# Optimization experiments

Measured on AMD Instinct MI355X. Metric: run time of the kernel, lower is better.

## Reference

```python
import jax, jax.numpy as jnp
import numpy as np

THRESHOLD = 16.0
BN_EPS = 1e-5


def setup_inputs() -> dict:
    key = jax.random.key(0)
    k_x, k_w, k_b, k_g, k_be = jax.random.split(key, 5)
    B, C, H, W = 4, 128, 64, 64
    C2 = 128
    x = jax.random.normal(k_x, (B, C, H, W), dtype=jnp.float32)
    # nn.Linear(c1, c2): weight [c2, c1], bias [c2]
    W_fc = jax.random.normal(k_w, (C2, C), dtype=jnp.float32) * (1.0 / np.sqrt(C))
    b_fc = jax.random.normal(k_b, (C2,), dtype=jnp.float32) * 0.01
    # BatchNorm2d affine params
    gamma = jnp.ones((C2,), dtype=jnp.float32) + 0.1 * jax.random.normal(k_g, (C2,), dtype=jnp.float32)
    beta = 0.1 * jax.random.normal(k_be, (C2,), dtype=jnp.float32)
    return {"x": x, "W_fc": W_fc, "b_fc": b_fc, "gamma": gamma, "beta": beta}


def reference(x, W_fc, b_fc, gamma, beta):
    b, c, h, w = x.shape
    xf = x.reshape(b, c, h * w).transpose(0, 2, 1)  # [B, N, C]

    # torch.cdist(feature, feature): pairwise L2 distances [B, N, N]
    sq = jnp.sum(xf * xf, axis=-1)  # [B, N]
    d2 = sq[:, :, None] + sq[:, None, :] - 2.0 * jnp.einsum('bic,bjc->bij', xf, xf)
    dist = jnp.sqrt(jnp.maximum(d2, 0.0))
    incidence = (dist < THRESHOLD).astype(x.dtype)  # [B, N, N], N vertices x N hyperedges

    # HyPConv: fc then vertex->edge (mean) then edge->vertex (mean)
    xe = jnp.einsum('bnc,dc->bnd', xf, W_fc) + b_fc  # [B, N, c2]

    # v2e: path = incidence^T (dims 1,2); mean over incident vertices
    deg_e = jnp.sum(incidence, axis=1)  # [B, N] = row-sums of incidence^T
    edge = jnp.einsum('bve,bvc->bec', incidence, xe)  # incidence^T @ xe
    edge = jnp.where(deg_e > 0, 1.0 / deg_e, 0.0)[:, :, None] * edge

    # e2v: path = incidence; mean over incident hyperedges
    deg_v = jnp.sum(incidence, axis=2)  # [B, N]
    vert = jnp.einsum('bve,bec->bvc', incidence, edge)
    vert = jnp.where(deg_v > 0, 1.0 / deg_v, 0.0)[:, :, None] * vert

    # residual is Identity (c1 == c2)
    out = vert + xf  # [B, N, c2]
    out = out.transpose(0, 2, 1).reshape(b, -1, h, w)  # [B, c2, H, W]

    # BatchNorm2d in training mode (batch statistics, biased variance)
    mean = jnp.mean(out, axis=(0, 2, 3))
    var = jnp.var(out, axis=(0, 2, 3))
    y = (out - mean[None, :, None, None]) * jax.lax.rsqrt(var[None, :, None, None] + BN_EPS)
    y = gamma[None, :, None, None] * y + beta[None, :, None, None]
    return y * jax.nn.sigmoid(y)  # SiLU
```

## Files before the change

kernel.cpp:

```cpp
#include <hip/hip_runtime.h>
#include <hip/hip_bf16.h>

#define NB 4
#define CH 128
#define NN 4096

typedef short bf16x8 __attribute__((ext_vector_type(8)));
typedef float f32x4 __attribute__((ext_vector_type(4)));
typedef float f32x16 __attribute__((ext_vector_type(16)));
using u16 = unsigned short;
using u32 = unsigned int;

__device__ __forceinline__ u16 f2bf(float v) {
  return __builtin_bit_cast(u16, __float2bfloat16(v));
}
__device__ __forceinline__ float bf2f(u16 u) {
  return __builtin_bit_cast(float, ((u32)u) << 16);
}

__device__ __forceinline__ void gld16(const void* g, void* l) {
  __builtin_amdgcn_global_load_lds((const __attribute__((address_space(1))) void*)g,
                                   (__attribute__((address_space(3))) void*)l,
                                   16, 0, 0);
}

__global__ void k_wbt(const float* __restrict__ W, u16* __restrict__ WbT) {
  int t = blockIdx.x * 256 + threadIdx.x;
  int c = t >> 7, d = t & 127;
  WbT[c * 128 + d] = f2bf(W[d * 128 + c]);
}

__global__ __launch_bounds__(256) void k_prep(const float* __restrict__ x,
                                              u16* __restrict__ xfb,
                                              float* __restrict__ sq) {
  __shared__ float ls[128][65];
  int blk = blockIdx.x;
  int b = blk >> 6;
  int n0 = (blk & 63) * 64;
  int t = threadIdx.x;
  const float* xb = x + (size_t)b * CH * NN;
  {
    int j = t & 63, cb = t >> 6;
#pragma unroll
    for (int i = 0; i < 32; ++i) {
      int c = cb * 32 + i;
      ls[c][j] = xb[(size_t)c * NN + n0 + j];
    }
  }
  __syncthreads();
  int jr = t >> 2, q = t & 3;
  float s = 0.f;
  u16* dst = xfb + ((size_t)b * NN + n0 + jr) * CH + q * 32;
#pragma unroll
  for (int ch = 0; ch < 4; ++ch) {
    u32 w[4];
#pragma unroll
    for (int p = 0; p < 4; ++p) {
      float va = ls[q * 32 + ch * 8 + 2 * p][jr];
      float vb = ls[q * 32 + ch * 8 + 2 * p + 1][jr];
      s += va * va + vb * vb;
      w[p] = (u32)f2bf(va) | ((u32)f2bf(vb) << 16);
    }
    ((uint4*)dst)[ch] = make_uint4(w[0], w[1], w[2], w[3]);
  }
  s += __shfl_xor(s, 1);
  s += __shfl_xor(s, 2);
  if (q == 0) sq[b * NN + n0 + jr] = s;
}

__global__ __launch_bounds__(256) void k_pack(const u16* __restrict__ xfb,
                                              const float* __restrict__ sq,
                                              u16* __restrict__ XA,
                                              u16* __restrict__ XG) {
  int bid = blockIdx.x;
  int b = bid >> 7, vt = bid & 127;
  int t = threadIdx.x;
  int v = t >> 3, q = t & 7;
  int row = vt * 32 + v;
  const u16* src = xfb + ((size_t)b * NN + row) * CH;
  size_t tb = ((size_t)b * 128 + vt) * 4608;
  float sv = sq[b * NN + row];
  u16 shi = f2bf(sv);
  u16 slo = f2bf(sv - bf2f(shi));
  const u32 one = 0x3F80u;
  for (int slot = q; slot < 18; slot += 8) {
    int k9 = slot >> 1, h = slot & 1;
    int dsto = (slot * 32 + v) * 8;
    uint4 pa, pg;
    if (k9 < 8) {
      pa = *(const uint4*)(src + k9 * 16 + h * 8);
      u32 w4[4] = {pa.x, pa.y, pa.z, pa.w};
      u32 g4[4];
#pragma unroll
      for (int p = 0; p < 4; ++p) {
        u16 lo = (u16)(w4[p] & 0xFFFF), hi16 = (u16)(w4[p] >> 16);
        u16 glo = f2bf(-2.f * bf2f(lo));
        u16 ghi = f2bf(-2.f * bf2f(hi16));
        g4[p] = (u32)glo | ((u32)ghi << 16);
      }
      pg = make_uint4(g4[0], g4[1], g4[2], g4[3]);
    } else {
      if (h == 0) {
        pa = make_uint4((u32)shi | ((u32)slo << 16), one | (one << 16), 0u, 0u);
        pg = make_uint4(one | (one << 16), (u32)shi | ((u32)slo << 16), 0u, 0u);
      } else {
        pa = make_uint4(0u, 0u, 0u, 0u);
        pg = pa;
      }
    }
    *(uint4*)(XA + tb + dsto) = pa;
    *(uint4*)(XG + tb + dsto) = pg;
  }
}

__global__ __launch_bounds__(256) void k_xe(const u16* __restrict__ xfb,
                                            const u16* __restrict__ WbT,
                                            const float* __restrict__ bfc,
                                            u16* __restrict__ XE2) {
  __shared__ char sm[65536];
  float* lsX = (float*)sm;
  u16* lsW = (u16*)(sm + 32768);
  int blk = blockIdx.x;  int b = blk >> 6;  int n0 = (blk & 63) * 64;
  int t = threadIdx.x;
  {
    int n = t >> 2, q = t & 3;
    const uint4* s4 = (const uint4*)(xfb + ((size_t)b * NN + n0 + n) * CH + q * 32);
    float* dstf = lsX + n * 128 + q * 32;
#pragma unroll
    for (int ch = 0; ch < 4; ++ch) {
      uint4 pk = s4[ch];
      u32 vals[4] = {pk.x, pk.y, pk.z, pk.w};
#pragma unroll
      for (int p = 0; p < 4; ++p) {
        dstf[ch * 8 + 2 * p]     = __builtin_bit_cast(float, vals[p] << 16);
        dstf[ch * 8 + 2 * p + 1] = __builtin_bit_cast(float, vals[p] & 0xFFFF0000u);
      }
    }
  }
  {
    int c = t >> 1, half = t & 1;
    const uint4* s = (const uint4*)(WbT + c * 128 + half * 64);
    uint4* d = (uint4*)(lsW + c * 128 + half * 64);
#pragma unroll
    for (int i = 0; i < 8; ++i) d[i] = s[i];
  }
  __syncthreads();
  int d = t & 127, ng = t >> 7;
  float acc[32];
  float bias = bfc[d];
#pragma unroll
  for (int n = 0; n < 32; ++n) acc[n] = bias;
  for (int c4 = 0; c4 < 32; ++c4) {
    float wv[4];
#pragma unroll
    for (int p = 0; p < 4; ++p) wv[p] = bf2f(lsW[(c4 * 4 + p) * 128 + d]);
#pragma unroll
    for (int n = 0; n < 32; ++n) {
      f32x4 xv = *(const f32x4*)(lsX + (ng * 32 + n) * 128 + c4 * 4);
      acc[n] = fmaf(xv[0], wv[0], acc[n]);
      acc[n] = fmaf(xv[1], wv[1], acc[n]);
      acc[n] = fmaf(xv[2], wv[2], acc[n]);
      acc[n] = fmaf(xv[3], wv[3], acc[n]);
    }
  }
  __syncthreads();
  u16* lsO = (u16*)sm;
#pragma unroll
  for (int n = 0; n < 32; ++n) lsO[d * 64 + ng * 32 + n] = f2bf(acc[n]);
  __syncthreads();
  {
    size_t tbv = ((size_t)b * 128 + (n0 >> 5));
#pragma unroll
    for (int it = 0; it < 4; ++it) {
      int cid = t + it * 256;
      int vtl = cid >> 9, g = cid & 511;
      int dloc = g & 31, hi2 = (g >> 5) & 1, h = (g >> 6) & 1, dt = g >> 7;
      int rowd = dt * 32 + dloc;
      int nl = vtl * 32 + h * 16 + hi2 * 8;
      *(uint4*)(XE2 + ((tbv + vtl) * 512 + g) * 8) = *(const uint4*)(lsO + rowd * 64 + nl);
    }
  }
}

__global__ __launch_bounds__(256, 2) void k_hyp(const u16* __restrict__ XAg,
                                                const u16* __restrict__ XGg,
                                                const u16* __restrict__ B2g,
                                                u16* __restrict__ outP,
                                                float* __restrict__ deg,
                                                int dodeg) {
  __shared__ __align__(16) char smem[34816];
  int t = threadIdx.x;
  int lane = t & 63, w = t >> 6;
  int r = lane & 31, hi = lane >> 5;
  int bid = blockIdx.x;
  int b = bid >> 7, rem = bid & 127;
  int et = rem >> 2, ks = rem & 3;
  int e0 = et * 128;
  int vt0 = ks * 32;

  bf16x8 B1[9];
  {
    const u16* g = XGg + ((size_t)(b * 128 + et * 4 + w)) * 4608 + (hi * 32 + r) * 8;
#pragma unroll
    for (int k9 = 0; k9 < 9; ++k9) B1[k9] = *(const bf16x8*)(g + k9 * 512);
  }

  f32x16 acc2[4];
#pragma unroll
  for (int dt = 0; dt < 4; ++dt)
#pragma unroll
    for (int q = 0; q < 16; ++q) acc2[dt][q] = 0.f;
  float dg = 0.f;

  const u16* xa_t = XAg + ((size_t)(b * 128 + vt0)) * 4608;
  const u16* b2_t = B2g + ((size_t)(b * 128 + vt0)) * 4096;

  {
    char* L = smem;
    for (int i = w; i < 9; i += 4) gld16(xa_t + i * 512 + lane * 8, L + i * 1024);
    for (int i = w; i < 8; i += 4) gld16(b2_t + i * 512 + lane * 8, L + 9216 + i * 1024);
  }
  __syncthreads();
  int cur = 0;
  for (int tile = 0; tile < 32; ++tile) {
    if (tile + 1 < 32) {
      char* L = smem + (cur ^ 1) * 17408;
      const u16* ga = xa_t + (size_t)(tile + 1) * 4608;
      const u16* gb = b2_t + (size_t)(tile + 1) * 4096;
      for (int i = w; i < 9; i += 4) gld16(ga + i * 512 + lane * 8, L + i * 1024);
      for (int i = w; i < 8; i += 4) gld16(gb + i * 512 + lane * 8, L + 9216 + i * 1024);
    }
    char* LA = smem + cur * 17408;
    char* LB = LA + 9216;
    f32x16 d2;
    {
      bf16x8 a1 = *(const bf16x8*)(LA + lane * 16);
      f32x16 z;
#pragma unroll
      for (int q = 0; q < 16; ++q) z[q] = 0.f;
      d2 = __builtin_amdgcn_mfma_f32_32x32x16_bf16(a1, B1[0], z, 0, 0, 0);
    }
#pragma unroll
    for (int k9 = 1; k9 < 9; ++k9) {
      bf16x8 a1 = *(const bf16x8*)(LA + k9 * 1024 + lane * 16);
      d2 = __builtin_amdgcn_mfma_f32_32x32x16_bf16(a1, B1[k9], d2, 0, 0, 0);
    }
    float p[16];
#pragma unroll
    for (int q = 0; q < 16; ++q) {
      p[q] = (d2[q] < 256.f) ? 1.f : 0.f;
      dg += p[q];
    }
    u32 c[8];
#pragma unroll
    for (int pr = 0; pr < 8; ++pr)
      asm("v_cvt_pk_bf16_f32 %0, %1, %2" : "=v"(c[pr]) : "v"(p[2 * pr]), "v"(p[2 * pr + 1]));
    asm volatile("v_permlane32_swap_b32 %0, %1" : "+v"(c[0]), "+v"(c[2]));
    asm volatile("v_permlane32_swap_b32 %0, %1" : "+v"(c[1]), "+v"(c[3]));
    asm volatile("v_permlane32_swap_b32 %0, %1" : "+v"(c[4]), "+v"(c[6]));
    asm volatile("v_permlane32_swap_b32 %0, %1" : "+v"(c[5]), "+v"(c[7]));
    uint4 u0 = make_uint4(c[0], c[1], c[2], c[3]);
    uint4 u1 = make_uint4(c[4], c[5], c[6], c[7]);
    bf16x8 A2h0 = __builtin_bit_cast(bf16x8, u0);
    bf16x8 A2h1 = __builtin_bit_cast(bf16x8, u1);
#pragma unroll
    for (int dt = 0; dt < 4; ++dt) {
      bf16x8 b20 = *(const bf16x8*)(LB + dt * 2048 + hi * 512 + r * 16);
      bf16x8 b21 = *(const bf16x8*)(LB + dt * 2048 + 1024 + hi * 512 + r * 16);
      acc2[dt] = __builtin_amdgcn_mfma_f32_32x32x16_bf16(A2h0, b20, acc2[dt], 0, 0, 0);
      acc2[dt] = __builtin_amdgcn_mfma_f32_32x32x16_bf16(A2h1, b21, acc2[dt], 0, 0, 0);
    }
    __syncthreads();
    cur ^= 1;
  }
  if (dodeg) {
    float dtot = dg + __shfl_xor(dg, 32);
    if (hi == 0) atomicAdd(&deg[b * NN + e0 + w * 32 + r], dtot);
  }
  {
    u16* lsE = (u16*)smem + w * 4096;
#pragma unroll
    for (int dt = 0; dt < 4; ++dt)
#pragma unroll
      for (int q = 0; q < 16; ++q) {
        int e_l = (q & 3) + 8 * (q >> 2) + 4 * hi;
        lsE[e_l * 128 + dt * 32 + r] = f2bf(acc2[dt][q]);
      }
  }
  __syncthreads();
  {
    uint4* g4 = (uint4*)(outP + ((size_t)(ks * NB + b) * NN + e0) * 128);
    const uint4* l4 = (const uint4*)smem;
#pragma unroll
    for (int i = 0; i < 8; ++i) g4[t + i * 256] = l4[t + i * 256];
  }
}

__global__ __launch_bounds__(256) void k_escale(const u16* __restrict__ P,
                                                const float* __restrict__ deg,
                                                u16* __restrict__ ED2) {
  int bid = blockIdx.x;
  int b = bid >> 7, et = bid & 127;
  int t = threadIdx.x;
#pragma unroll
  for (int c2 = 0; c2 < 2; ++c2) {
    int g = t + c2 * 256;
    int dloc = g & 31, hi2 = (g >> 5) & 1, h = (g >> 6) & 1, dt = g >> 7;
    int d = dt * 32 + dloc;
    int ebase = et * 32 + h * 16 + hi2 * 8;
    u16 outv[8];
#pragma unroll
    for (int j = 0; j < 8; ++j) {
      int e = ebase + j;
      size_t idx = ((size_t)b * NN + e) * 128 + d;
      float s = bf2f(P[idx]) + bf2f(P[idx + 2097152]) +
                bf2f(P[idx + 2 * 2097152]) + bf2f(P[idx + 3 * 2097152]);
      float dv = deg[b * NN + e];
      float f = dv > 0.f ? 1.0f / dv : 0.f;
      outv[j] = f2bf(s * f);
    }
    *(uint4*)(ED2 + (((size_t)b * 128 + et) * 512 + g) * 8) = *(uint4*)outv;
  }
}

__global__ __launch_bounds__(256) void k_vfin(const u16* __restrict__ P,
                                              const float* __restrict__ deg,
                                              const float* __restrict__ x,
                                              float* __restrict__ outp,
                                              float* __restrict__ bnsum,
                                              float* __restrict__ bnsq) {
  __shared__ float lsT[128][72];
  int blk = blockIdx.x;  int b = blk >> 6;  int n0 = (blk & 63) * 64;
  int t = threadIdx.x;
  {
    int n = t >> 2, q = t & 3;
    int i = n0 + n;
    float dv = deg[b * NN + i];
    float f = dv > 0.f ? 1.0f / dv : 0.f;
    size_t base = ((size_t)b * NN + i) * 128 + q * 32;
    float vs[32];
#pragma unroll
    for (int j = 0; j < 32; ++j) vs[j] = 0.f;
#pragma unroll
    for (int kss = 0; kss < 4; ++kss) {
      const u16* src = P + (size_t)kss * 2097152 + base;
#pragma unroll
      for (int ch = 0; ch < 4; ++ch) {
        uint4 pk = *(const uint4*)(src + ch * 8);
        u32 wv[4] = {pk.x, pk.y, pk.z, pk.w};
#pragma unroll
        for (int pp = 0; pp < 4; ++pp) {
          vs[ch * 8 + 2 * pp]     += bf2f((u16)(wv[pp] & 0xFFFF));
          vs[ch * 8 + 2 * pp + 1] += bf2f((u16)(wv[pp] >> 16));
        }
      }
    }
#pragma unroll
    for (int j = 0; j < 32; ++j) lsT[q * 32 + j][n] = vs[j] * f;
  }
  __syncthreads();
  {
    int d = t >> 1, half = t & 1;
    const float* xr = x + ((size_t)b * CH + d) * NN + n0 + half * 32;
    float* orow = outp + ((size_t)b * CH + d) * NN + n0 + half * 32;
    float s = 0.f, s2 = 0.f;
#pragma unroll
    for (int i = 0; i < 32; ++i) {
      float v = lsT[d][half * 32 + i] + xr[i];
      orow[i] = v;
      s += v;  s2 += v * v;
    }
    s += __shfl_xor(s, 1);
    s2 += __shfl_xor(s2, 1);
    if (half == 0) { atomicAdd(&bnsum[d], s); atomicAdd(&bnsq[d], s2); }
  }
}

__global__ void k_bn(float* __restrict__ y, const float* __restrict__ bnsum,
                     const float* __restrict__ bnsq, const float* __restrict__ gamma,
                     const float* __restrict__ beta) {
  int idx = blockIdx.x * 256 + threadIdx.x;
  int d = (idx >> 12) & 127;
  const float cnt = (float)(NB * NN);
  float m = bnsum[d] / cnt;
  float var = bnsq[d] / cnt - m * m;
  float rs = rsqrtf(var + 1e-5f);
  float v = y[idx];
  float tt = (v - m) * rs * gamma[d] + beta[d];
  y[idx] = tt / (1.0f + expf(-tt));
}

extern "C" void kernel_launch(void* const* d_in, const int* in_sizes, int n_in,
                              void* d_out, int out_size, void* d_ws, size_t ws_size,
                              hipStream_t stream) {
  (void)in_sizes; (void)n_in; (void)out_size; (void)ws_size;
  const float* x     = (const float*)d_in[0];
  const float* W     = (const float*)d_in[1];
  const float* bfc   = (const float*)d_in[2];
  const float* gamma = (const float*)d_in[3];
  const float* beta  = (const float*)d_in[4];
  char* ws = (char*)d_ws;
  u16* Pbuf  = (u16*)ws;
  u16* XA    = (u16*)(ws + 16777216);
  u16* XG    = (u16*)(ws + 21495808);
  u16* XE2   = (u16*)(ws + 26214400);
  u16* ED2   = (u16*)(ws + 30408704);
  u16* xfb   = (u16*)(ws + 34603008);
  u16* WbT   = (u16*)(ws + 38797312);
  float* sqb = (float*)(ws + 38830080);
  float* deg = (float*)(ws + 38895616);
  float* bnsum = (float*)(ws + 38961152);
  float* bnsq  = (float*)(ws + 38961664);

  hipMemsetAsync(ws + 38895616, 0, 66560, stream);
  k_wbt<<<64, 256, 0, stream>>>(W, WbT);
  k_prep<<<NB * 64, 256, 0, stream>>>(x, xfb, sqb);
  k_pack<<<NB * 128, 256, 0, stream>>>(xfb, sqb, XA, XG);
  k_xe<<<NB * 64, 256, 0, stream>>>(xfb, WbT, bfc, XE2);
  k_hyp<<<512, 256, 0, stream>>>(XA, XG, XE2, Pbuf, deg, 1);
  k_escale<<<NB * 128, 256, 0, stream>>>(Pbuf, deg, ED2);
  k_hyp<<<512, 256, 0, stream>>>(XA, XG, ED2, Pbuf, deg, 0);
  k_vfin<<<NB * 64, 256, 0, stream>>>(Pbuf, deg, x, (float*)d_out, bnsum, bnsq);
  k_bn<<<2097152 / 256, 256, 0, stream>>>((float*)d_out, bnsum, bnsq, gamma, beta);
}
```

Measured before the change: 202.7 us.

## Fuse prep/pack, use MFMA for fc, split hyp over 8 K-slices

Merges the transpose, squared-norm and packing kernels into one k_prep that writes the XA/XG MFMA tiles directly, and drops the separate weight-transpose kernel. Rewrites the fc projection with bf16 MFMA instructions. Splits the hypergraph kernel's reduction into 8 slices instead of 4 with higher occupancy and two independent MFMA accumulator chains. It also templates the mode and writes edge partials in the tiled layout so k_escale reads them with coalesced accesses. The intent is fewer launches, more parallel blocks and less serial MFMA dependency, at the cost of a larger partial buffer and more reduction traffic in escale and vfin.

```diff
diff --git a/kernel.cpp b/kernel.cpp
--- a/kernel.cpp
+++ b/kernel.cpp
@@ -4,6 +4,7 @@
 #define NB 4
 #define CH 128
 #define NN 4096
+#define KS 8
 
 typedef short bf16x8 __attribute__((ext_vector_type(8)));
 typedef float f32x4 __attribute__((ext_vector_type(4)));
@@ -17,6 +18,9 @@
 __device__ __forceinline__ float bf2f(u16 u) {
   return __builtin_bit_cast(float, ((u32)u) << 16);
 }
+__device__ __forceinline__ u32 pk2(float a, float b) {
+  return (u32)f2bf(a) | ((u32)f2bf(b) << 16);
+}
 
 __device__ __forceinline__ void gld16(const void* g, void* l) {
   __builtin_amdgcn_global_load_lds((const __attribute__((address_space(1))) void*)g,
@@ -24,16 +28,11 @@
                                    16, 0, 0);
 }
 
-__global__ void k_wbt(const float* __restrict__ W, u16* __restrict__ WbT) {
-  int t = blockIdx.x * 256 + threadIdx.x;
-  int c = t >> 7, d = t & 127;
-  WbT[c * 128 + d] = f2bf(W[d * 128 + c]);
-}
-
 __global__ __launch_bounds__(256) void k_prep(const float* __restrict__ x,
-                                              u16* __restrict__ xfb,
-                                              float* __restrict__ sq) {
+                                              u16* __restrict__ XA,
+                                              u16* __restrict__ XG) {
   __shared__ float ls[128][65];
+  __shared__ float sqs[64];
   int blk = blockIdx.x;
   int b = blk >> 6;
   int n0 = (blk & 63) * 64;
@@ -48,155 +47,121 @@
     }
   }
   __syncthreads();
-  int jr = t >> 2, q = t & 3;
-  float s = 0.f;
-  u16* dst = xfb + ((size_t)b * NN + n0 + jr) * CH + q * 32;
-#pragma unroll
-  for (int ch = 0; ch < 4; ++ch) {
-    u32 w[4];
-#pragma unroll
-    for (int p = 0; p < 4; ++p) {
-      float va = ls[q * 32 + ch * 8 + 2 * p][jr];
-      float vb = ls[q * 32 + ch * 8 + 2 * p + 1][jr];
-      s += va * va + vb * vb;
-      w[p] = (u32)f2bf(va) | ((u32)f2bf(vb) << 16);
-    }
-    ((uint4*)dst)[ch] = make_uint4(w[0], w[1], w[2], w[3]);
-  }
-  s += __shfl_xor(s, 1);
-  s += __shfl_xor(s, 2);
-  if (q == 0) sq[b * NN + n0 + jr] = s;
-}
-
-__global__ __launch_bounds__(256) void k_pack(const u16* __restrict__ xfb,
-                                              const float* __restrict__ sq,
-                                              u16* __restrict__ XA,
-                                              u16* __restrict__ XG) {
-  int bid = blockIdx.x;
-  int b = bid >> 7, vt = bid & 127;
-  int t = threadIdx.x;
-  int v = t >> 3, q = t & 7;
-  int row = vt * 32 + v;
-  const u16* src = xfb + ((size_t)b * NN + row) * CH;
-  size_t tb = ((size_t)b * 128 + vt) * 4608;
-  float sv = sq[b * NN + row];
-  u16 shi = f2bf(sv);
-  u16 slo = f2bf(sv - bf2f(shi));
-  const u32 one = 0x3F80u;
-  for (int slot = q; slot < 18; slot += 8) {
-    int k9 = slot >> 1, h = slot & 1;
-    int dsto = (slot * 32 + v) * 8;
-    uint4 pa, pg;
-    if (k9 < 8) {
-      pa = *(const uint4*)(src + k9 * 16 + h * 8);
-      u32 w4[4] = {pa.x, pa.y, pa.z, pa.w};
-      u32 g4[4];
-#pragma unroll
-      for (int p = 0; p < 4; ++p) {
-        u16 lo = (u16)(w4[p] & 0xFFFF), hi16 = (u16)(w4[p] >> 16);
-        u16 glo = f2bf(-2.f * bf2f(lo));
-        u16 ghi = f2bf(-2.f * bf2f(hi16));
-        g4[p] = (u32)glo | ((u32)ghi << 16);
+  if (t < 64) {
+    float s = 0.f;
+#pragma unroll
+    for (int c = 0; c < 128; ++c) { float v = ls[c][t]; s += v * v; }
+    sqs[t] = s;
+  }
+  __syncthreads();
+  int v = t & 31, g = t >> 5;
+  const u32 one2 = 0x3F803F80u;
+#pragma unroll
+  for (int vt2 = 0; vt2 < 2; ++vt2) {
+    int j = vt2 * 32 + v;
+    float sv = sqs[j];
+    u16 shi = f2bf(sv);
+    u16 slo = f2bf(sv - bf2f(shi));
+    size_t tb = ((size_t)b * 128 + (n0 >> 5) + vt2) * 4608;
+    for (int s = g; s < 18; s += 8) {
+      int k9 = s >> 1, h = s & 1;
+      int c0 = k9 * 16 + h * 8;
+      u32 wa[4], wg[4];
+      if (k9 < 8) {
+#pragma unroll
+        for (int p = 0; p < 4; ++p) {
+          float va = ls[c0 + 2 * p][j], vb = ls[c0 + 2 * p + 1][j];
+          wa[p] = pk2(va, vb);
+          wg[p] = pk2(-2.f * va, -2.f * vb);
+        }
+      } else if (h == 0) {
+        wa[0] = (u32)shi | ((u32)slo << 16); wa[1] = one2; wa[2] = 0u; wa[3] = 0u;
+        wg[0] = one2; wg[1] = (u32)shi | ((u32)slo << 16); wg[2] = 0u; wg[3] = 0u;
+      } else {
+        wa[0] = wa[1] = wa[2] = wa[3] = 0u;
+        wg[0] = wg[1] = wg[2] = wg[3] = 0u;
       }
-      pg = make_uint4(g4[0], g4[1], g4[2], g4[3]);
-    } else {
-      if (h == 0) {
-        pa = make_uint4((u32)shi | ((u32)slo << 16), one | (one << 16), 0u, 0u);
-        pg = make_uint4(one | (one << 16), (u32)shi | ((u32)slo << 16), 0u, 0u);
-      } else {
-        pa = make_uint4(0u, 0u, 0u, 0u);
-        pg = pa;
-      }
-    }
-    *(uint4*)(XA + tb + dsto) = pa;
-    *(uint4*)(XG + tb + dsto) = pg;
-  }
-}
-
-__global__ __launch_bounds__(256) void k_xe(const u16* __restrict__ xfb,
-                                            const u16* __restrict__ WbT,
+      *(uint4*)(XA + tb + (size_t)s * 256 + v * 8) = make_uint4(wa[0], wa[1], wa[2], wa[3]);
+      *(uint4*)(XG + tb + (size_t)s * 256 + v * 8) = make_uint4(wg[0], wg[1], wg[2], wg[3]);
+    }
+  }
+}
+
+__global__ __launch_bounds__(256) void k_xe(const u16* __restrict__ XA,
+                                            const float* __restrict__ W,
                                             const float* __restrict__ bfc,
                                             u16* __restrict__ XE2) {
-  __shared__ char sm[65536];
-  float* lsX = (float*)sm;
-  u16* lsW = (u16*)(sm + 32768);
-  int blk = blockIdx.x;  int b = blk >> 6;  int n0 = (blk & 63) * 64;
+  __shared__ __align__(16) char sw[32768];
   int t = threadIdx.x;
-  {
-    int n = t >> 2, q = t & 3;
-    const uint4* s4 = (const uint4*)(xfb + ((size_t)b * NN + n0 + n) * CH + q * 32);
-    float* dstf = lsX + n * 128 + q * 32;
-#pragma unroll
-    for (int ch = 0; ch < 4; ++ch) {
-      uint4 pk = s4[ch];
-      u32 vals[4] = {pk.x, pk.y, pk.z, pk.w};
-#pragma unroll
-      for (int p = 0; p < 4; ++p) {
-        dstf[ch * 8 + 2 * p]     = __builtin_bit_cast(float, vals[p] << 16);
-        dstf[ch * 8 + 2 * p + 1] = __builtin_bit_cast(float, vals[p] & 0xFFFF0000u);
+  int lane = t & 63, w = t >> 6;
+  int r = lane & 31, hi = lane >> 5;
+  int b = blockIdx.x >> 5, nt = blockIdx.x & 31;
+  int vt = nt * 4 + w;
+  {
+    int d = t >> 1, half = t & 1;
+    const float4* src = (const float4*)(W + (size_t)d * 128 + half * 64);
+    int rowoff = d * 256, sz = (d & 7) << 4;
+#pragma unroll
+    for (int ch = 0; ch < 8; ++ch) {
+      float4 f0 = src[ch * 2], f1 = src[ch * 2 + 1];
+      *(uint4*)(sw + ((rowoff + half * 128 + ch * 16) ^ sz)) =
+          make_uint4(pk2(f0.x, f0.y), pk2(f0.z, f0.w), pk2(f1.x, f1.y), pk2(f1.z, f1.w));
+    }
+  }
+  float bias[4];
+#pragma unroll
+  for (int dt = 0; dt < 4; ++dt) bias[dt] = bfc[dt * 32 + r];
+  __syncthreads();
+  const u16* abase = XA + ((size_t)(b * 128 + vt)) * 4608;
+  bf16x8 a[8];
+#pragma unroll
+  for (int k9 = 0; k9 < 8; ++k9)
+    a[k9] = *(const bf16x8*)(abase + (k9 * 2 + hi) * 256 + r * 8);
+  f32x16 acc[4];
+#pragma unroll
+  for (int dt = 0; dt < 4; ++dt)
+#pragma unroll
+    for (int q = 0; q < 16; ++q) acc[dt][q] = bias[dt];
+#pragma unroll
+  for (int k9 = 0; k9 < 8; ++k9) {
+#pragma unroll
+    for (int dt = 0; dt < 4; ++dt) {
+      int d = dt * 32 + r;
+      bf16x8 bf_ = *(const bf16x8*)(sw + ((d * 256 + k9 * 32 + hi * 16) ^ ((d & 7) << 4)));
+      acc[dt] = __builtin_amdgcn_mfma_f32_32x32x16_bf16(a[k9], bf_, acc[dt], 0, 0, 0);
+    }
+  }
+  u16* base = XE2 + ((size_t)(b * 128 + vt)) * 4096;
+#pragma unroll
+  for (int dt = 0; dt < 4; ++dt)
+#pragma unroll
+    for (int h = 0; h < 2; ++h)
+#pragma unroll
+      for (int hi2 = 0; hi2 < 2; ++hi2) {
+        int q0 = h * 8 + hi2 * 4;
+        u32 w0 = pk2(acc[dt][q0], acc[dt][q0 + 1]);
+        u32 w1 = pk2(acc[dt][q0 + 2], acc[dt][q0 + 3]);
+        *(uint2*)(base + (((dt * 2 + h) * 2 + hi2) * 32 + r) * 8 + hi * 4) =
+            make_uint2(w0, w1);
       }
-    }
-  }
-  {
-    int c = t >> 1, half = t & 1;
-    const uint4* s = (const uint4*)(WbT + c * 128 + half * 64);
-    uint4* d = (uint4*)(lsW + c * 128 + half * 64);
-#pragma unroll
-    for (int i = 0; i < 8; ++i) d[i] = s[i];
-  }
-  __syncthreads();
-  int d = t & 127, ng = t >> 7;
-  float acc[32];
-  float bias = bfc[d];
-#pragma unroll
-  for (int n = 0; n < 32; ++n) acc[n] = bias;
-  for (int c4 = 0; c4 < 32; ++c4) {
-    float wv[4];
-#pragma unroll
-    for (int p = 0; p < 4; ++p) wv[p] = bf2f(lsW[(c4 * 4 + p) * 128 + d]);
-#pragma unroll
-    for (int n = 0; n < 32; ++n) {
-      f32x4 xv = *(const f32x4*)(lsX + (ng * 32 + n) * 128 + c4 * 4);
-      acc[n] = fmaf(xv[0], wv[0], acc[n]);
-      acc[n] = fmaf(xv[1], wv[1], acc[n]);
-      acc[n] = fmaf(xv[2], wv[2], acc[n]);
-      acc[n] = fmaf(xv[3], wv[3], acc[n]);
-    }
-  }
-  __syncthreads();
-  u16* lsO = (u16*)sm;
-#pragma unroll
-  for (int n = 0; n < 32; ++n) lsO[d * 64 + ng * 32 + n] = f2bf(acc[n]);
-  __syncthreads();
-  {
-    size_t tbv = ((size_t)b * 128 + (n0 >> 5));
-#pragma unroll
-    for (int it = 0; it < 4; ++it) {
-      int cid = t + it * 256;
-      int vtl = cid >> 9, g = cid & 511;
-      int dloc = g & 31, hi2 = (g >> 5) & 1, h = (g >> 6) & 1, dt = g >> 7;
-      int rowd = dt * 32 + dloc;
-      int nl = vtl * 32 + h * 16 + hi2 * 8;
-      *(uint4*)(XE2 + ((tbv + vtl) * 512 + g) * 8) = *(const uint4*)(lsO + rowd * 64 + nl);
-    }
-  }
-}
-
-__global__ __launch_bounds__(256, 2) void k_hyp(const u16* __restrict__ XAg,
+}
+
+template <int MODE>
+__global__ __launch_bounds__(256, 4) void k_hyp(const u16* __restrict__ XAg,
                                                 const u16* __restrict__ XGg,
                                                 const u16* __restrict__ B2g,
                                                 u16* __restrict__ outP,
-                                                float* __restrict__ deg,
-                                                int dodeg) {
+                                                float* __restrict__ deg) {
   __shared__ __align__(16) char smem[34816];
   int t = threadIdx.x;
   int lane = t & 63, w = t >> 6;
   int r = lane & 31, hi = lane >> 5;
   int bid = blockIdx.x;
-  int b = bid >> 7, rem = bid & 127;
-  int et = rem >> 2, ks = rem & 3;
+  int b = bid >> 8;
+  int et = (bid >> 3) & 31;
+  int ks = bid & 7;
   int e0 = et * 128;
-  int vt0 = ks * 32;
+  int vt0 = ks * 16;
 
   bf16x8 B1[9];
   {
@@ -211,6 +176,9 @@
 #pragma unroll
     for (int q = 0; q < 16; ++q) acc2[dt][q] = 0.f;
   float dg = 0.f;
+  f32x16 zero;
+#pragma unroll
+  for (int q = 0; q < 16; ++q) zero[q] = 0.f;
 
   const u16* xa_t = XAg + ((size_t)(b * 128 + vt0)) * 4608;
   const u16* b2_t = B2g + ((size_t)(b * 128 + vt0)) * 4096;
@@ -222,8 +190,8 @@
   }
   __syncthreads();
   int cur = 0;
-  for (int tile = 0; tile < 32; ++tile) {
-    if (tile + 1 < 32) {
+  for (int tile = 0; tile < 16; ++tile) {
+    if (tile + 1 < 16) {
       char* L = smem + (cur ^ 1) * 17408;
       const u16* ga = xa_t + (size_t)(tile + 1) * 4608;
       const u16* gb = b2_t + (size_t)(tile + 1) * 4096;
@@ -232,23 +200,25 @@
     }
     char* LA = smem + cur * 17408;
     char* LB = LA + 9216;
-    f32x16 d2;
+    f32x16 d2a, d2b;
     {
-      bf16x8 a1 = *(const bf16x8*)(LA + lane * 16);
-      f32x16 z;
-#pragma unroll
-      for (int q = 0; q < 16; ++q) z[q] = 0.f;
-      d2 = __builtin_amdgcn_mfma_f32_32x32x16_bf16(a1, B1[0], z, 0, 0, 0);
-    }
-#pragma unroll
-    for (int k9 = 1; k9 < 9; ++k9) {
-      bf16x8 a1 = *(const bf16x8*)(LA + k9 * 1024 + lane * 16);
-      d2 = __builtin_amdgcn_mfma_f32_32x32x16_bf16(a1, B1[k9], d2, 0, 0, 0);
+      bf16x8 a0 = *(const bf16x8*)(LA + lane * 16);
+      bf16x8 a1 = *(const bf16x8*)(LA + 1024 + lane * 16);
+      d2a = __builtin_amdgcn_mfma_f32_32x32x16_bf16(a0, B1[0], zero, 0, 0, 0);
+      d2b = __builtin_amdgcn_mfma_f32_32x32x16_bf16(a1, B1[1], zero, 0, 0, 0);
+    }
+#pragma unroll
+    for (int k9 = 2; k9 < 9; ++k9) {
+      bf16x8 av = *(const bf16x8*)(LA + k9 * 1024 + lane * 16);
+      if (k9 & 1)
+        d2b = __builtin_amdgcn_mfma_f32_32x32x16_bf16(av, B1[k9], d2b, 0, 0, 0);
+      else
+        d2a = __builtin_amdgcn_mfma_f32_32x32x16_bf16(av, B1[k9], d2a, 0, 0, 0);
     }
     float p[16];
 #pragma unroll
     for (int q = 0; q < 16; ++q) {
-      p[q] = (d2[q] < 256.f) ? 1.f : 0.f;
+      p[q] = ((d2a[q] + d2b[q]) < 256.f) ? 1.f : 0.f;
       dg += p[q];
     }
     u32 c[8];
@@ -273,11 +243,23 @@
     __syncthreads();
     cur ^= 1;
   }
-  if (dodeg) {
+  if (MODE == 0) {
     float dtot = dg + __shfl_xor(dg, 32);
     if (hi == 0) atomicAdd(&deg[b * NN + e0 + w * 32 + r], dtot);
-  }
-  {
+    u16* base = outP + ((size_t)(ks * NB + b) * 128 + (et * 4 + w)) * 4096;
+#pragma unroll
+    for (int dt = 0; dt < 4; ++dt)
+#pragma unroll
+      for (int h = 0; h < 2; ++h)
+#pragma unroll
+        for (int hi2 = 0; hi2 < 2; ++hi2) {
+          int q0 = h * 8 + hi2 * 4;
+          u32 w0 = pk2(acc2[dt][q0], acc2[dt][q0 + 1]);
+          u32 w1 = pk2(acc2[dt][q0 + 2], acc2[dt][q0 + 3]);
+          *(uint2*)(base + (((dt * 2 + h) * 2 + hi2) * 32 + r) * 8 + hi * 4) =
+              make_uint2(w0, w1);
+        }
+  } else {
     u16* lsE = (u16*)smem + w * 4096;
 #pragma unroll
     for (int dt = 0; dt < 4; ++dt)
@@ -286,9 +268,7 @@
         int e_l = (q & 3) + 8 * (q >> 2) + 4 * hi;
         lsE[e_l * 128 + dt * 32 + r] = f2bf(acc2[dt][q]);
       }
-  }
-  __syncthreads();
-  {
+    __syncthreads();
     uint4* g4 = (uint4*)(outP + ((size_t)(ks * NB + b) * NN + e0) * 128);
     const uint4* l4 = (const uint4*)smem;
 #pragma unroll
@@ -296,30 +276,42 @@
   }
 }
 
-__global__ __launch_bounds__(256) void k_escale(const u16* __restrict__ P,
+__global__ __launch_bounds__(256) void k_escale(const u16* __restrict__ PA,
                                                 const float* __restrict__ deg,
                                                 u16* __restrict__ ED2) {
-  int bid = blockIdx.x;
-  int b = bid >> 7, et = bid & 127;
-  int t = threadIdx.x;
-#pragma unroll
-  for (int c2 = 0; c2 < 2; ++c2) {
-    int g = t + c2 * 256;
-    int dloc = g & 31, hi2 = (g >> 5) & 1, h = (g >> 6) & 1, dt = g >> 7;
-    int d = dt * 32 + dloc;
-    int ebase = et * 32 + h * 16 + hi2 * 8;
-    u16 outv[8];
-#pragma unroll
-    for (int j = 0; j < 8; ++j) {
-      int e = ebase + j;
-      size_t idx = ((size_t)b * NN + e) * 128 + d;
-      float s = bf2f(P[idx]) + bf2f(P[idx + 2097152]) +
-                bf2f(P[idx + 2 * 2097152]) + bf2f(P[idx + 3 * 2097152]);
-      float dv = deg[b * NN + e];
-      float f = dv > 0.f ? 1.0f / dv : 0.f;
-      outv[j] = f2bf(s * f);
-    }
-    *(uint4*)(ED2 + (((size_t)b * 128 + et) * 512 + g) * 8) = *(uint4*)outv;
+  int m = blockIdx.x * 256 + threadIdx.x;
+#pragma unroll
+  for (int it = 0; it < 2; ++it, m += 131072) {
+    int g = m & 511, vt = (m >> 9) & 127, b = m >> 16;
+    int hi2 = (g >> 5) & 1, h = (g >> 6) & 1;
+    int e0 = vt * 32 + h * 16 + hi2 * 8;
+    float4 dg0 = *(const float4*)(deg + b * NN + e0);
+    float4 dg1 = *(const float4*)(deg + b * NN + e0 + 4);
+    float s[8];
+#pragma unroll
+    for (int j = 0; j < 8; ++j) s[j] = 0.f;
+    size_t off = ((size_t)(b * 128 + vt) * 512 + g) * 8;
+#pragma unroll
+    for (int ksv = 0; ksv < KS; ++ksv) {
+      uint4 pkv = *(const uint4*)(PA + (size_t)ksv * 2097152 + off);
+      u32 wv[4] = {pkv.x, pkv.y, pkv.z, pkv.w};
+#pragma unroll
+      for (int p = 0; p < 4; ++p) {
+        s[2 * p]     += bf2f((u16)(wv[p] & 0xFFFF));
+        s[2 * p + 1] += bf2f((u16)(wv[p] >> 16));
+      }
+    }
+    float iv[8];
+    iv[0] = dg0.x; iv[1] = dg0.y; iv[2] = dg0.z; iv[3] = dg0.w;
+    iv[4] = dg1.x; iv[5] = dg1.y; iv[6] = dg1.z; iv[7] = dg1.w;
+    u32 o[4];
+#pragma unroll
+    for (int p = 0; p < 4; ++p) {
+      float f0 = iv[2 * p]     > 0.f ? s[2 * p]     / iv[2 * p]     : 0.f;
+      float f1 = iv[2 * p + 1] > 0.f ? s[2 * p + 1] / iv[2 * p + 1] : 0.f;
+      o[p] = pk2(f0, f1);
+    }
+    *(uint4*)(ED2 + off) = make_uint4(o[0], o[1], o[2], o[3]);
   }
 }
 
@@ -341,13 +333,12 @@
     float vs[32];
 #pragma unroll
     for (int j = 0; j < 32; ++j) vs[j] = 0.f;
-#pragma unroll
-    for (int kss = 0; kss < 4; ++kss) {
+    for (int kss = 0; kss < KS; ++kss) {
       const u16* src = P + (size_t)kss * 2097152 + base;
 #pragma unroll
       for (int ch = 0; ch < 4; ++ch) {
-        uint4 pk = *(const uint4*)(src + ch * 8);
-        u32 wv[4] = {pk.x, pk.y, pk.z, pk.w};
+        uint4 pkv = *(const uint4*)(src + ch * 8);
+        u32 wv[4] = {pkv.x, pkv.y, pkv.z, pkv.w};
 #pragma unroll
         for (int pp = 0; pp < 4; ++pp) {
           vs[ch * 8 + 2 * pp]     += bf2f((u16)(wv[pp] & 0xFFFF));
@@ -401,25 +392,20 @@
   const float* beta  = (const float*)d_in[4];
   char* ws = (char*)d_ws;
   u16* Pbuf  = (u16*)ws;
-  u16* XA    = (u16*)(ws + 16777216);
-  u16* XG    = (u16*)(ws + 21495808);
-  u16* XE2   = (u16*)(ws + 26214400);
-  u16* ED2   = (u16*)(ws + 30408704);
-  u16* xfb   = (u16*)(ws + 34603008);
-  u16* WbT   = (u16*)(ws + 38797312);
-  float* sqb = (float*)(ws + 38830080);
-  float* deg = (float*)(ws + 38895616);
-  float* bnsum = (float*)(ws + 38961152);
-  float* bnsq  = (float*)(ws + 38961664);
-
-  hipMemsetAsync(ws + 38895616, 0, 66560, stream);
-  k_wbt<<<64, 256, 0, stream>>>(W, WbT);
-  k_prep<<<NB * 64, 256, 0, stream>>>(x, xfb, sqb);
-  k_pack<<<NB * 128, 256, 0, stream>>>(xfb, sqb, XA, XG);
-  k_xe<<<NB * 64, 256, 0, stream>>>(xfb, WbT, bfc, XE2);
-  k_hyp<<<512, 256, 0, stream>>>(XA, XG, XE2, Pbuf, deg, 1);
-  k_escale<<<NB * 128, 256, 0, stream>>>(Pbuf, deg, ED2);
-  k_hyp<<<512, 256, 0, stream>>>(XA, XG, ED2, Pbuf, deg, 0);
+  u16* XA    = (u16*)(ws + 33554432);
+  u16* XG    = (u16*)(ws + 38273024);
+  u16* XE2   = (u16*)(ws + 42991616);
+  u16* ED2   = (u16*)(ws + 47185920);
+  float* deg = (float*)(ws + 51380224);
+  float* bnsum = (float*)(ws + 51445760);
+  float* bnsq  = (float*)(ws + 51446272);
+
+  hipMemsetAsync(ws + 51380224, 0, 66560, stream);
+  k_prep<<<NB * 64, 256, 0, stream>>>(x, XA, XG);
+  k_xe<<<NB * 32, 256, 0, stream>>>(XA, W, bfc, XE2);
+  k_hyp<0><<<NB * 32 * KS, 256, 0, stream>>>(XA, XG, XE2, Pbuf, deg);
+  k_escale<<<512, 256, 0, stream>>>(Pbuf, deg, ED2);
+  k_hyp<1><<<NB * 32 * KS, 256, 0, stream>>>(XA, XG, ED2, Pbuf, deg);
   k_vfin<<<NB * 64, 256, 0, stream>>>(Pbuf, deg, x, (float*)d_out, bnsum, bnsq);
   k_bn<<<2097152 / 256, 256, 0, stream>>>((float*)d_out, bnsum, bnsq, gamma, beta);
 }
```

Measured after the change: 245.5 us. 1.21x slower.
